# Performance work log

Hardware: AMD Instinct MI355X
Metric: run time of the kernel (lower is better)

The kernel has to match this reference:

```python
import jax, jax.numpy as jnp
import numpy as np

N, A, AD, D, H, KTOP = 5, 900, 8, 256, 8, 300


def _bbox_min_max(anchor):
    # anchor: [N,A,8] = x,y,z,logw,logl,logh,sin_yaw,cos_yaw
    xyz = anchor[..., :3]
    w, l, h = [jnp.exp(anchor[..., i]) for i in (3, 4, 5)]
    sy, cy = anchor[..., 6], anchor[..., 7]
    yaw = jnp.arctan2(sy, cy)
    ca, sa = jnp.abs(jnp.cos(yaw)), jnp.abs(jnp.sin(yaw))
    ex = 0.5 * (l * ca + w * sa)
    ey = 0.5 * (l * sa + w * ca)
    half = jnp.stack([ex, ey, 0.5 * h], axis=-1)
    return xyz - half, xyz + half


def _forward(i2j_anchor, b_anchor, b_feature, transform_matrix, anchor_embed,
             w_roi, b_roi, bn_g, bn_b, fc1_w, fc1_b, fc2_w, fc2_b,
             anc_w, anc_b, lam_w, lam_b, wq, bq, wk, bk, wv, bv, wo, bo,
             ln_g, ln_b, K):
    n, a, ad = b_anchor.shape
    d = b_feature.shape[-1]
    heads = lam_w.shape[-1]
    dh = d // heads
    # ROI scoring + topk selection of anchors to broadcast to neighbors
    roi = jax.nn.sigmoid(b_feature @ w_roi + b_roi)[..., 0]              # [N,A]
    top_scores, top_idx = jax.lax.top_k(roi, K)                          # [N,K]
    conf = top_scores > 0.5                                              # [N,K]
    nbr = jnp.take_along_axis(b_feature, top_idx[..., None], axis=1)     # [N,K,D]
    idx4 = jnp.broadcast_to(top_idx[None, :, :, None], (n, n, K, ad))
    i2j_sel = jnp.take_along_axis(i2j_anchor, idx4, axis=2)              # [N,N,K,AD]
    # remove self (eye-mask): off-diagonal j per row i, row-major order
    offdiag = np.array([[j for j in range(n) if j != i] for i in range(n)])
    rows = np.arange(n)[:, None]
    m = K * (n - 1)
    i2j_rm = i2j_sel[rows, offdiag].reshape(n, m, ad)                    # [N,M,AD]
    tm_rm = transform_matrix[rows, offdiag]                              # [N,N-1,4,4]
    key_feat = nbr[offdiag].reshape(n, m, d)                             # [N,M,D]
    conf_rm = conf[offdiag].reshape(n, m, 1)
    nf_masked = key_feat * conf_rm
    # bbox-range masked aggregation of neighbor features into ego anchors
    mn, mx = _bbox_min_max(b_anchor)                                     # [N,A,3]
    centers = i2j_rm[..., :3]                                            # [N,M,3]
    inside = jnp.all((centers[:, None, :, :] >= mn[:, :, None, :]) &
                     (centers[:, None, :, :] <= mx[:, :, None, :]), axis=-1)  # [N,A,M]
    agg = jnp.einsum('nam,nmd->nad', inside.astype(b_feature.dtype), nf_masked)
    is_greater_than_range = ~jnp.any(inside, axis=1)                     # [N,M]
    b_feature = b_feature + agg
    # transform-matrix encoding: first 3 rows of 4x4 -> BN -> MLP
    mlp_in = tm_rm[:, :, :3, :].reshape(-1, 12)
    mu = mlp_in.mean(0)
    var = mlp_in.var(0)
    xbn = (mlp_in - mu) / jnp.sqrt(var + 1e-5) * bn_g + bn_b
    t = jax.nn.relu(xbn @ fc1_w + fc1_b) @ fc2_w + fc2_b                 # [N*(N-1),D]
    trans_enc = jnp.repeat(t.reshape(n, n - 1, 1, d), K, axis=2).reshape(n, m, d)
    key_pos = i2j_rm @ anc_w + anc_b + trans_enc                         # anchorencoder + trans
    # distance-biased attention mask
    diff = b_anchor[:, :, None, :2] - i2j_rm[:, None, :, :2]
    dist = jnp.sqrt(jnp.sum(diff * diff, axis=-1) + 1e-12)               # cdist [N,A,M]
    lm = (b_feature @ lam_w + lam_b).transpose(0, 2, 1)                  # [N,H,A]
    bias = -jnp.log1p(dist)[:, None, :, :] * lm[..., None]               # [N,H,A,M]
    # multi-head attention (query=b_feature(+anchor_embed pos), key/value=neighbors)
    q = b_feature + anchor_embed
    k = key_feat + key_pos
    v = key_feat
    qh = (q @ wq + bq).reshape(n, a, heads, dh)
    kh = (k @ wk + bk).reshape(n, m, heads, dh)
    vh = (v @ wv + bv).reshape(n, m, heads, dh)
    logits = jnp.einsum('nahd,nmhd->nham', qh, kh) / np.sqrt(dh).astype(np.float32) + bias
    attn = jax.nn.softmax(logits, axis=-1)
    out = jnp.einsum('nham,nmhd->nahd', attn, vh).reshape(n, a, d) @ wo + bo
    res = b_feature + out                                                # residual (identity=query)
    mu2 = res.mean(-1, keepdims=True)
    var2 = res.var(-1, keepdims=True)
    return (res - mu2) / jnp.sqrt(var2 + 1e-5) * ln_g + ln_b


def setup_inputs() -> dict:
    key = jax.random.key(0)
    ks = jax.random.split(key, 24)
    s = 0.05
    inp = {
        'i2j_anchor': jax.random.normal(ks[0], (N, N, A, AD), jnp.float32),
        'b_anchor': jax.random.normal(ks[1], (N, A, AD), jnp.float32),
        'b_feature': jax.random.normal(ks[2], (N, A, D), jnp.float32),
        'transform_matrix': jax.random.normal(ks[3], (N, N, 4, 4), jnp.float32),
        'anchor_embed': jax.random.normal(ks[4], (N, A, D), jnp.float32),
        'w_roi': jax.random.normal(ks[5], (D, 1), jnp.float32) * s,
        'b_roi': jnp.zeros((1,), jnp.float32),
        'bn_g': jnp.ones((12,), jnp.float32),
        'bn_b': jnp.zeros((12,), jnp.float32),
        'fc1_w': jax.random.normal(ks[6], (12, D), jnp.float32) * s,
        'fc1_b': jnp.zeros((D,), jnp.float32),
        'fc2_w': jax.random.normal(ks[7], (D, D), jnp.float32) * s,
        'fc2_b': jnp.zeros((D,), jnp.float32),
        'anc_w': jax.random.normal(ks[8], (AD, D), jnp.float32) * s,
        'anc_b': jnp.zeros((D,), jnp.float32),
        'lam_w': jax.random.normal(ks[9], (D, H), jnp.float32) * s,
        'lam_b': jnp.zeros((H,), jnp.float32),
        'wq': jax.random.normal(ks[10], (D, D), jnp.float32) * s,
        'bq': jnp.zeros((D,), jnp.float32),
        'wk': jax.random.normal(ks[11], (D, D), jnp.float32) * s,
        'bk': jnp.zeros((D,), jnp.float32),
        'wv': jax.random.normal(ks[12], (D, D), jnp.float32) * s,
        'bv': jnp.zeros((D,), jnp.float32),
        'wo': jax.random.normal(ks[13], (D, D), jnp.float32) * s,
        'bo': jnp.zeros((D,), jnp.float32),
        'ln_g': jnp.ones((D,), jnp.float32),
        'ln_b': jnp.zeros((D,), jnp.float32),
        'K': KTOP,
    }
    return inp


def reference(i2j_anchor, b_anchor, b_feature, transform_matrix, anchor_embed,
              w_roi, b_roi, bn_g, bn_b, fc1_w, fc1_b, fc2_w, fc2_b,
              anc_w, anc_b, lam_w, lam_b, wq, bq, wk, bk, wv, bv, wo, bo,
              ln_g, ln_b, K):
    return _forward(i2j_anchor, b_anchor, b_feature, transform_matrix, anchor_embed,
                    w_roi, b_roi, bn_g, bn_b, fc1_w, fc1_b, fc2_w, fc2_b,
                    anc_w, anc_b, lam_w, lam_b, wq, bq, wk, bk, wv, bv, wo, bo,
                    ln_g, ln_b, K)
```

## Files before the change

kernel.cpp:

```cpp
#include <hip/hip_runtime.h>
#include <math.h>

#define N_ 5
#define A_ 900
#define AD_ 8
#define D_ 256
#define H_ 8
#define DH_ 32
#define K_ 300
#define NM1_ 4
#define M_ 1200
#define MP_ 1216
#define KC_ 64
#define HALF_ 600
#define NCHUNK2_ 10

typedef _Float16 f16x8 __attribute__((ext_vector_type(8)));
typedef _Float16 f16x4 __attribute__((ext_vector_type(4)));
typedef float f32x4 __attribute__((ext_vector_type(4)));

__global__ __launch_bounds__(256) void score_kernel(const float* __restrict__ bf,
                                                    const float* __restrict__ w,
                                                    const float* __restrict__ b,
                                                    float* __restrict__ scores) {
  int wid = threadIdx.x >> 6, lane = threadIdx.x & 63;
  int row = blockIdx.x * 4 + wid;
  if (row >= N_ * A_) return;
  const float* x = bf + (long)row * D_;
  float dot = 0.f;
#pragma unroll
  for (int t = 0; t < 4; t++) dot += x[lane + 64 * t] * w[lane + 64 * t];
#pragma unroll
  for (int o = 32; o; o >>= 1) dot += __shfl_xor(dot, o, 64);
  if (lane == 0) scores[row] = 1.0f / (1.0f + expf(-(dot + b[0])));
}

__global__ __launch_bounds__(1024) void topk_kernel(const float* __restrict__ scores,
                                                    int* __restrict__ top_idx,
                                                    float* __restrict__ conf) {
  __shared__ float sc[1024];
  __shared__ int si[1024];
  int i = blockIdx.x, t = threadIdx.x;
  sc[t] = (t < A_) ? scores[i * A_ + t] : -INFINITY;
  si[t] = t;
  __syncthreads();
  for (int k = 2; k <= 1024; k <<= 1) {
    for (int j = k >> 1; j > 0; j >>= 1) {
      int ixj = t ^ j;
      if (ixj > t) {
        bool dir = ((t & k) == 0);
        float a = sc[t], b = sc[ixj];
        bool sw = dir ? (a < b) : (a > b);
        if (sw) {
          sc[t] = b; sc[ixj] = a;
          int tmp = si[t]; si[t] = si[ixj]; si[ixj] = tmp;
        }
      }
      __syncthreads();
    }
  }
  if (t < K_) {
    top_idx[i * K_ + t] = si[t];
    conf[i * K_ + t] = sc[t] > 0.5f ? 1.0f : 0.0f;
  }
}

__global__ __launch_bounds__(256) void mlp_kernel(const float* __restrict__ tm,
                                                  const float* __restrict__ bn_g, const float* __restrict__ bn_b,
                                                  const float* __restrict__ fc1_w, const float* __restrict__ fc1_b,
                                                  const float* __restrict__ fc2_w, const float* __restrict__ fc2_b,
                                                  float* __restrict__ t_out) {
  int r = blockIdx.x;
  int t = threadIdx.x;
  __shared__ float x[20][12];
  __shared__ float y[12];
  __shared__ float hbuf[D_];
  if (t < 240) {
    int rr = t / 12, f = t % 12;
    int i = rr / NM1_, jj = rr % NM1_;
    int j = jj < i ? jj : jj + 1;
    int r4 = f / 4, c4 = f % 4;
    x[rr][f] = tm[((long)(i * N_ + j) * 4 + r4) * 4 + c4];
  }
  __syncthreads();
  if (t < 12) {
    float s = 0.f;
    for (int rr = 0; rr < 20; rr++) s += x[rr][t];
    float m = s / 20.0f;
    float v = 0.f;
    for (int rr = 0; rr < 20; rr++) { float d = x[rr][t] - m; v += d * d; }
    v /= 20.0f;
    y[t] = (x[r][t] - m) * rsqrtf(v + 1e-5f) * bn_g[t] + bn_b[t];
  }
  __syncthreads();
  float acc = fc1_b[t];
#pragma unroll
  for (int f = 0; f < 12; f++) acc += y[f] * fc1_w[f * D_ + t];
  hbuf[t] = fmaxf(acc, 0.0f);
  __syncthreads();
  float acc2 = fc2_b[t];
  for (int k = 0; k < D_; k++) acc2 += hbuf[k] * fc2_w[k * D_ + t];
  t_out[r * D_ + t] = acc2;
}

#define GKT_ 10
__global__ __launch_bounds__(256) void gather_kernel(const float* __restrict__ b_feature,
                                                     const float* __restrict__ i2j_anchor,
                                                     const int* __restrict__ top_idx,
                                                     const float* __restrict__ conf,
                                                     const float* __restrict__ anc_w,
                                                     const float* __restrict__ anc_b,
                                                     const float* __restrict__ t_mlp,
                                                     _Float16* __restrict__ key_feat16,
                                                     float* __restrict__ conf_rm,
                                                     float* __restrict__ i2j_rm,
                                                     _Float16* __restrict__ key_in16) {
  int blk = blockIdx.x;
  int i = blk / NM1_, jj = blk % NM1_;
  int j = jj < i ? jj : jj + 1;
  int k0 = blockIdx.y * GKT_;
  int c = threadIdx.x;
  __shared__ float aw[AD_][D_];
#pragma unroll
  for (int r = 0; r < AD_; r++) aw[r][c] = anc_w[r * D_ + c];
  float ab = anc_b[c];
  float tv = t_mlp[(i * NM1_ + jj) * D_ + c];
  __syncthreads();
  for (int k = k0; k < k0 + GKT_; k++) {
    int idx = top_idx[j * K_ + k];
    float cf = conf[j * K_ + k];
    const float* src = b_feature + ((long)(j * A_ + idx)) * D_;
    float val = src[c];
    long mrow = (long)i * M_ + jj * K_ + k;
    key_feat16[mrow * D_ + c] = (_Float16)val;
    const float* ap = i2j_anchor + ((long)((i * N_ + j) * A_ + idx)) * AD_;
    if (c < AD_) i2j_rm[mrow * AD_ + c] = ap[c];
    if (c == 0) conf_rm[mrow] = cf;
    float pos = ab + tv;
#pragma unroll
    for (int r = 0; r < AD_; r++) pos += ap[r] * aw[r][c];
    key_in16[mrow * D_ + c] = (_Float16)(val + pos);
  }
}

__global__ __launch_bounds__(256) void trans_kernel(const float* __restrict__ w0, const float* __restrict__ w1,
                                                    const float* __restrict__ w2, const float* __restrict__ w3,
                                                    const _Float16* __restrict__ kf,
                                                    _Float16* __restrict__ wT, _Float16* __restrict__ kT) {
  int bid = blockIdx.x;
  int t = threadIdx.x;
  if (bid < 64) {
    int y = bid >> 4, tile = bid & 15;
    const float* src = (y == 0) ? w0 : (y == 1) ? w1 : (y == 2) ? w2 : w3;
    _Float16* dst = wT + (size_t)y * D_ * D_;
    int kr = (tile >> 2) * 64, nc = (tile & 3) * 64;
    __shared__ float lds[64][65];
#pragma unroll
    for (int r = 0; r < 16; r++) {
      int row = r * 4 + (t >> 6), col = t & 63;
      lds[row][col] = src[(size_t)(kr + row) * D_ + nc + col];
    }
    __syncthreads();
#pragma unroll
    for (int r = 0; r < 16; r++) {
      int orow = r * 4 + (t >> 6), ocol = t & 63;
      dst[(size_t)(nc + orow) * D_ + kr + ocol] = (_Float16)lds[ocol][orow];
    }
  } else {
    int b = bid - 64;
    int i = b / 76, rem = b % 76;
    int m0 = (rem % 19) * 64, d0 = (rem / 19) * 64;
    __shared__ _Float16 lds2[64][66];
    const _Float16* src = kf + (size_t)i * M_ * D_;
    _Float16* dst = kT + (size_t)i * D_ * M_;
#pragma unroll
    for (int r = 0; r < 16; r++) {
      int row = r * 4 + (t >> 6), col = t & 63;
      int m = m0 + row;
      lds2[row][col] = (m < M_) ? src[(size_t)m * D_ + d0 + col] : (_Float16)0.0f;
    }
    __syncthreads();
#pragma unroll
    for (int r = 0; r < 16; r++) {
      int orow = r * 4 + (t >> 6), ocol = t & 63;
      int m = m0 + ocol;
      if (m < M_) dst[(size_t)(d0 + orow) * M_ + m] = lds2[ocol][orow];
    }
  }
}

__global__ __launch_bounds__(256) void insbias_kernel(const float* __restrict__ i2j_rm,
                                                      const float* __restrict__ conf_rm,
                                                      const float* __restrict__ ban,
                                                      _Float16* __restrict__ inside,
                                                      _Float16* __restrict__ Lbuf) {
  int i = blockIdx.x;
  int g = blockIdx.y;
  __shared__ float cx[M_], cy[M_], cz[M_], cf[M_];
  for (int m = threadIdx.x; m < M_; m += 256) {
    const float* cp = i2j_rm + ((long)i * M_ + m) * AD_;
    cx[m] = cp[0]; cy[m] = cp[1]; cz[m] = cp[2];
    cf[m] = conf_rm[(long)i * M_ + m];
  }
  __syncthreads();
#pragma unroll
  for (int r = 0; r < 4; r++) {
    int a = g * 4 + r;
    int row = i * A_ + a;
    const float* ap = ban + (long)row * AD_;
    float ax = ap[0], ay = ap[1], az = ap[2];
    float w = expf(ap[3]), l = expf(ap[4]), hh = expf(ap[5]);
    float yaw = atan2f(ap[6], ap[7]);
    float ca = fabsf(cosf(yaw)), sa = fabsf(sinf(yaw));
    float ex = 0.5f * (l * ca + w * sa);
    float ey = 0.5f * (l * sa + w * ca);
    float ez = 0.5f * hh;
    float mn0 = ax - ex, mn1 = ay - ey, mn2 = az - ez;
    float mx0 = ax + ex, mx1 = ay + ey, mx2 = az + ez;
    _Float16* ldst = Lbuf + (size_t)row * MP_;
    _Float16* idst = inside + (size_t)row * M_;
    for (int m = threadIdx.x; m < M_; m += 256) {
      float c0 = cx[m], c1 = cy[m], c2 = cz[m];
      bool ins = (c0 >= mn0) && (c0 <= mx0) && (c1 >= mn1) && (c1 <= mx1) && (c2 >= mn2) && (c2 <= mx2);
      idst[m] = ins ? (_Float16)cf[m] : (_Float16)0.0f;
      float dx = ax - c0, dy = ay - c1;
      ldst[m] = (_Float16)log1pf(sqrtf(dx * dx + dy * dy + 1e-12f));
    }
  }
}

#define GLD_ 74
template <typename TO, bool HAS_BIAS, bool HAS_RES>
__device__ __forceinline__ void gemm_tile_body(
    const _Float16* __restrict__ A, int lda, int Mr,
    const _Float16* __restrict__ B, int ldb,
    const float* __restrict__ bias, const float* __restrict__ res,
    TO* __restrict__ C, int ldc,
    int m0, int n0, int k_begin, int k_end) {
  __shared__ _Float16 As[64 * GLD_];
  __shared__ _Float16 Bs[64 * GLD_];
  int tid = threadIdx.x;
  int lane = tid & 63;
  int wid = tid >> 6;
  int wr = (wid >> 1) * 32, wc = (wid & 1) * 32;
  int lr = lane & 15, lk = (lane >> 4) * 8;
  int srow = tid >> 3;
  int scol = (tid & 7) * 8;
  f16x8 aR[2], bR[2];
  f16x8 zero8 = {};
  auto loadg = [&](int kb) {
#pragma unroll
    for (int r = 0; r < 2; r++) {
      int gm = m0 + srow + r * 32;
      int gk = kb + scol;
      aR[r] = (gm < Mr && gk < k_end) ? *(const f16x8*)&A[(size_t)gm * lda + gk] : zero8;
      int gn = n0 + srow + r * 32;
      bR[r] = (gk < k_end) ? *(const f16x8*)&B[(size_t)gn * ldb + gk] : zero8;
    }
  };
  auto store_lds = [&]() {
#pragma unroll
    for (int r = 0; r < 2; r++) {
      *(f16x8*)&As[(srow + r * 32) * GLD_ + scol] = aR[r];
      *(f16x8*)&Bs[(srow + r * 32) * GLD_ + scol] = bR[r];
    }
  };
  f32x4 acc[2][2] = {};
  int niter = (k_end - k_begin + 63) >> 6;
  loadg(k_begin);
  store_lds();
  __syncthreads();
  for (int it = 0; it < niter; ++it) {
    bool more = (it + 1 < niter);
    if (more) loadg(k_begin + (it + 1) * 64);
#pragma unroll
    for (int ks = 0; ks < 2; ks++) {
      f16x8 af[2], bf[2];
#pragma unroll
      for (int mi = 0; mi < 2; mi++) af[mi] = *(const f16x8*)&As[(wr + mi * 16 + lr) * GLD_ + ks * 32 + lk];
#pragma unroll
      for (int ni = 0; ni < 2; ni++) bf[ni] = *(const f16x8*)&Bs[(wc + ni * 16 + lr) * GLD_ + ks * 32 + lk];
#pragma unroll
      for (int mi = 0; mi < 2; mi++)
#pragma unroll
        for (int ni = 0; ni < 2; ni++)
          acc[mi][ni] = __builtin_amdgcn_mfma_f32_16x16x32_f16(af[mi], bf[ni], acc[mi][ni], 0, 0, 0);
    }
    __syncthreads();
    if (more) { store_lds(); __syncthreads(); }
  }
#pragma unroll
  for (int mi = 0; mi < 2; mi++)
#pragma unroll
    for (int ni = 0; ni < 2; ni++)
#pragma unroll
      for (int rr = 0; rr < 4; rr++) {
        int row = m0 + wr + mi * 16 + (lane >> 4) * 4 + rr;
        int col = n0 + wc + ni * 16 + lr;
        if (row < Mr) {
          float v = acc[mi][ni][rr];
          if (HAS_BIAS) v += bias[col];
          if (HAS_RES) v += res[(size_t)row * ldc + col];
          C[(size_t)row * ldc + col] = (TO)v;
        }
      }
}

__global__ __launch_bounds__(256) void agg_kernel(const _Float16* __restrict__ inside16,
                                                  const _Float16* __restrict__ kT16,
                                                  float* __restrict__ partial) {
  int i = blockIdx.z >> 2, sk = blockIdx.z & 3;
  int kb = sk * 320;
  int ke = kb + 320 < M_ ? kb + 320 : M_;
  gemm_tile_body<float, false, false>(
      inside16 + (size_t)i * A_ * M_, M_, A_,
      kT16 + (size_t)i * D_ * M_, M_,
      nullptr, nullptr,
      partial + (size_t)(sk * N_ + i) * A_ * D_, D_,
      blockIdx.x * 64, blockIdx.y * 64, kb, ke);
}

__global__ __launch_bounds__(256) void agg_reduce(const float* __restrict__ partial,
                                                  const float* __restrict__ b_feature,
                                                  const float* __restrict__ anchor_embed,
                                                  const float* __restrict__ lam_w,
                                                  const float* __restrict__ lam_b,
                                                  float* __restrict__ bf_upd,
                                                  _Float16* __restrict__ qin16,
                                                  float* __restrict__ lm_rm) {
  int wid = threadIdx.x >> 6, lane = threadIdx.x & 63;
  int rg = blockIdx.x * 4 + wid;
  int d0 = lane * 4;
  float lw[4][8];
#pragma unroll
  for (int e = 0; e < 4; e++) {
#pragma unroll
    for (int h = 0; h < 8; h++) lw[e][h] = lam_w[(d0 + e) * 8 + h];
  }
  float4 s = *(const float4*)&partial[(size_t)rg * D_ + d0];
#pragma unroll
  for (int sk = 1; sk < 4; sk++) {
    float4 p = *(const float4*)&partial[((size_t)sk * N_ * A_ + rg) * D_ + d0];
    s.x += p.x; s.y += p.y; s.z += p.z; s.w += p.w;
  }
  float4 bf = *(const float4*)&b_feature[(size_t)rg * D_ + d0];
  s.x += bf.x; s.y += bf.y; s.z += bf.z; s.w += bf.w;
  *(float4*)&bf_upd[(size_t)rg * D_ + d0] = s;
  float4 ae = *(const float4*)&anchor_embed[(size_t)rg * D_ + d0];
  f16x4 q4;
  q4[0] = (_Float16)(s.x + ae.x); q4[1] = (_Float16)(s.y + ae.y);
  q4[2] = (_Float16)(s.z + ae.z); q4[3] = (_Float16)(s.w + ae.w);
  *(f16x4*)&qin16[(size_t)rg * D_ + d0] = q4;
  float sv[4] = {s.x, s.y, s.z, s.w};
  float acc[8] = {};
#pragma unroll
  for (int e = 0; e < 4; e++)
#pragma unroll
    for (int h = 0; h < 8; h++) acc[h] += sv[e] * lw[e][h];
#pragma unroll
  for (int h = 0; h < 8; h++) {
#pragma unroll
    for (int o = 32; o; o >>= 1) acc[h] += __shfl_xor(acc[h], o, 64);
  }
  if (lane == 0) {
#pragma unroll
    for (int h = 0; h < 8; h++) lm_rm[(size_t)rg * H_ + h] = acc[h] + lam_b[h];
  }
}

__global__ __launch_bounds__(256) void qkv_kernel(const _Float16* __restrict__ qA,
                                                  const _Float16* __restrict__ kA,
                                                  const _Float16* __restrict__ vA,
                                                  const _Float16* __restrict__ wT,
                                                  const float* __restrict__ bq,
                                                  const float* __restrict__ bk,
                                                  const float* __restrict__ bv,
                                                  _Float16* __restrict__ qC,
                                                  _Float16* __restrict__ kC,
                                                  _Float16* __restrict__ vC) {
  int bid = blockIdx.x;
  const _Float16 *Ap, *Bp;
  const float* bias;
  _Float16* Cp;
  int Mr, t, mt, nt;
  if (bid < 284)      { Ap = qA; Bp = wT;               bias = bq; Cp = qC; Mr = 4500; t = bid;       mt = t % 71; nt = t / 71; }
  else if (bid < 660) { Ap = kA; Bp = wT + D_ * D_;     bias = bk; Cp = kC; Mr = 6000; t = bid - 284; mt = t % 94; nt = t / 94; }
  else                { Ap = vA; Bp = wT + 2 * D_ * D_; bias = bv; Cp = vC; Mr = 6000; t = bid - 660; mt = t % 94; nt = t / 94; }
  gemm_tile_body<_Float16, true, false>(Ap, D_, Mr, Bp, D_, bias, nullptr, Cp, D_, mt * 64, nt * 64, 0, D_);
}

__global__ __launch_bounds__(256) void outp_kernel(const _Float16* __restrict__ att16,
                                                   const _Float16* __restrict__ woT,
                                                   float* __restrict__ partial2) {
  int bid = blockIdx.x;
  int sk = bid >= 284 ? 1 : 0;
  int t = bid - sk * 284;
  int mt = t % 71, nt = t / 71;
  gemm_tile_body<float, false, false>(att16, D_, 4500, woT, D_, nullptr, nullptr,
                                      partial2 + (size_t)sk * 4500 * D_, D_,
                                      mt * 64, nt * 64, sk * 128, sk * 128 + 128);
}

#define LQP_ 72
#define LKS_ 40
__global__ __launch_bounds__(256) void attn_mfma(const _Float16* __restrict__ qh16,
                                                 const _Float16* __restrict__ kh16,
                                                 const _Float16* __restrict__ vh16,
                                                 const float* __restrict__ lm_rm,
                                                 const _Float16* __restrict__ Lbuf,
                                                 float* __restrict__ part_ms,
                                                 float* __restrict__ part_o) {
  int bid = blockIdx.x;
  int wgid = (bid & 7) * 150 + (bid >> 3);
  int ih = wgid / 30;
  int rest = wgid % 30;
  int half = rest / 15, qt = rest % 15;
  int i = ih >> 3, h = ih & 7;
  int a0 = qt * 64;
  int mbase = half * HALF_;
  int mlimit = mbase + HALF_;

  __shared__ _Float16 QP[64 * LQP_];
  __shared__ _Float16 Ks[64 * LKS_];
  __shared__ _Float16 Vt[32][74];
  __shared__ _Float16 Ls[64 * LQP_];
  __shared__ float lmvs[64];

  int tid = threadIdx.x;
  int lane = tid & 63;
  int w16 = (tid >> 6) * 16;
  int lr = lane & 15;
  int lk = (lane >> 4) * 8;
  int mq = (lane >> 4) * 4;
  int srow = tid >> 2, spiece = tid & 3;
  int lrow = tid >> 3, lpc = (tid & 7) * 8;

  {
    int aq = a0 + srow;
    int a_ld = aq < A_ ? aq : A_ - 1;
    const uint4* src = (const uint4*)(qh16 + ((long)(i * A_ + a_ld) * D_ + h * DH_));
    *(uint4*)&QP[srow * LQP_ + spiece * 8] = src[spiece];
  }
  if (tid < 64) {
    int aq = a0 + tid;
    int a_ld = aq < A_ ? aq : A_ - 1;
    lmvs[tid] = lm_rm[(long)(i * A_ + a_ld) * H_ + h];
  }

  const _Float16* kb = kh16 + (long)i * M_ * D_ + h * DH_;
  const _Float16* vb = vh16 + (long)i * M_ * D_ + h * DH_;
  const _Float16* lptr[2];
#pragma unroll
  for (int rr = 0; rr < 2; rr++) {
    int aq = a0 + lrow + rr * 32;
    int a_ld = aq < A_ ? aq : A_ - 1;
    lptr[rr] = Lbuf + (size_t)(i * A_ + a_ld) * MP_ + lpc;
  }

  uint4 kvR, vvR;
  f16x8 lR[2];
  auto loadr = [&](int c) {
    int m0 = mbase + c * KC_;
    int mrow = m0 + srow;
    if (mrow < M_) {
      kvR = ((const uint4*)(kb + (long)mrow * D_))[spiece];
      vvR = ((const uint4*)(vb + (long)mrow * D_))[spiece];
    } else {
      kvR = make_uint4(0, 0, 0, 0);
      vvR = make_uint4(0, 0, 0, 0);
    }
#pragma unroll
    for (int rr = 0; rr < 2; rr++) lR[rr] = *(const f16x8*)&lptr[rr][m0];
  };

  __syncthreads();

  int qrow = w16 + lr;
  float lmv = lmvs[qrow];
  f16x8 qa = *(const f16x8*)&QP[qrow * LQP_ + lk];

  float m_run = -INFINITY, s_part = 0.0f;
  f32x4 oacc[2] = {};

  loadr(0);

  for (int c = 0; c < NCHUNK2_; c++) {
    int m0 = mbase + c * KC_;
    __syncthreads();
    *(uint4*)&Ks[srow * LKS_ + spiece * 8] = kvR;
    {
      const _Float16* hp = (const _Float16*)&vvR;
#pragma unroll
      for (int e = 0; e < 8; e++) Vt[spiece * 8 + e][srow] = hp[e];
    }
#pragma unroll
    for (int rr = 0; rr < 2; rr++) *(f16x8*)&Ls[(lrow + rr * 32) * LQP_ + lpc] = lR[rr];
    if (c + 1 < NCHUNK2_) loadr(c + 1);
    __syncthreads();

    f32x4 sacc[4];
#pragma unroll
    for (int mb = 0; mb < 4; mb++) {
      f16x8 kf = *(const f16x8*)&Ks[(mb * 16 + lr) * LKS_ + lk];
      sacc[mb] = __builtin_amdgcn_mfma_f32_16x16x32_f16(kf, qa, (f32x4){0.f, 0.f, 0.f, 0.f}, 0, 0, 0);
    }

    float lg[4][4];
#pragma unroll
    for (int mb = 0; mb < 4; mb++) {
      f16x4 l4 = *(const f16x4*)&Ls[qrow * LQP_ + mb * 16 + mq];
#pragma unroll
      for (int rr = 0; rr < 4; rr++) {
        int mcol = m0 + mb * 16 + mq + rr;
        float v = sacc[mb][rr] * 0.17677669529663687f - (float)l4[rr] * lmv;
        lg[mb][rr] = (mcol < mlimit) ? v : -INFINITY;
      }
    }
    float cm = -INFINITY;
#pragma unroll
    for (int mb = 0; mb < 4; mb++)
#pragma unroll
      for (int rr = 0; rr < 4; rr++) cm = fmaxf(cm, lg[mb][rr]);
    cm = fmaxf(cm, __shfl_xor(cm, 16, 64));
    cm = fmaxf(cm, __shfl_xor(cm, 32, 64));
    float nm = fmaxf(m_run, cm);
    float corr = __expf(m_run - nm);
    m_run = nm;
    float ps = 0.0f;
#pragma unroll
    for (int mb = 0; mb < 4; mb++) {
      f16x4 p4;
#pragma unroll
      for (int rr = 0; rr < 4; rr++) {
        float p = __expf(lg[mb][rr] - nm);
        ps += p;
        p4[rr] = (_Float16)p;
      }
      *(f16x4*)&QP[qrow * LQP_ + mb * 16 + mq] = p4;
    }
    s_part = s_part * corr + ps;
#pragma unroll
    for (int r = 0; r < 4; r++) {
      float cr = __shfl(corr, (lane & 48) + mq + r, 64);
      oacc[0][r] *= cr;
      oacc[1][r] *= cr;
    }

#pragma unroll
    for (int ks = 0; ks < 2; ks++) {
      f16x8 pa = *(const f16x8*)&QP[(w16 + lr) * LQP_ + ks * 32 + lk];
#pragma unroll
      for (int db = 0; db < 2; db++) {
        f16x8 vf = *(const f16x8*)&Vt[db * 16 + lr][ks * 32 + lk];
        oacc[db] = __builtin_amdgcn_mfma_f32_16x16x32_f16(pa, vf, oacc[db], 0, 0, 0);
      }
    }
  }

  float st = s_part;
  st += __shfl_xor(st, 16, 64);
  st += __shfl_xor(st, 32, 64);

  size_t base = (size_t)(half * 40 + ih) * A_;
  if (lane < 16) {
    int a = a0 + w16 + lane;
    if (a < A_) {
      part_ms[(base + a) * 2 + 0] = m_run;
      part_ms[(base + a) * 2 + 1] = st;
    }
  }
#pragma unroll
  for (int r = 0; r < 4; r++) {
    int a = a0 + w16 + mq + r;
    if (a < A_) {
      size_t rowb = base + a;
      part_o[rowb * 32 + lr] = oacc[0][r];
      part_o[rowb * 32 + 16 + lr] = oacc[1][r];
    }
  }
}

__global__ __launch_bounds__(256) void attn_merge(const float* __restrict__ part_ms,
                                                  const float* __restrict__ part_o,
                                                  _Float16* __restrict__ att16) {
  int t = threadIdx.x;
  int R = blockIdx.x * 8 + (t >> 5);
  int d = t & 31;
  int ih = R / A_, a = R % A_;
  int i = ih >> 3, h = ih & 7;
  size_t r0 = (size_t)ih * A_ + a;
  size_t r1 = (size_t)(40 + ih) * A_ + a;
  float m0 = part_ms[r0 * 2], s0 = part_ms[r0 * 2 + 1];
  float m1 = part_ms[r1 * 2], s1 = part_ms[r1 * 2 + 1];
  float M = fmaxf(m0, m1);
  float e0 = __expf(m0 - M), e1 = __expf(m1 - M);
  float inv = 1.0f / (s0 * e0 + s1 * e1);
  float o = part_o[r0 * 32 + d] * e0 + part_o[r1 * 32 + d] * e1;
  att16[((size_t)(i * A_ + a)) * D_ + h * DH_ + d] = (_Float16)(o * inv);
}

__global__ __launch_bounds__(256) void ln_kernel(const float* __restrict__ partial2,
                                                 const float* __restrict__ bo,
                                                 const float* __restrict__ resid,
                                                 const float* __restrict__ g,
                                                 const float* __restrict__ b,
                                                 float* __restrict__ out) {
  int row = blockIdx.x;
  int t = threadIdx.x;
  size_t idx = (size_t)row * D_ + t;
  float v = partial2[idx] + partial2[(size_t)4500 * D_ + idx] + bo[t] + resid[idx];
  float s = v, sq = v * v;
#pragma unroll
  for (int o = 32; o; o >>= 1) {
    s += __shfl_xor(s, o, 64);
    sq += __shfl_xor(sq, o, 64);
  }
  __shared__ float ss[4], ssq[4];
  int wid = t >> 6, lane = t & 63;
  if (lane == 0) { ss[wid] = s; ssq[wid] = sq; }
  __syncthreads();
  float ts = ss[0] + ss[1] + ss[2] + ss[3];
  float tq = ssq[0] + ssq[1] + ssq[2] + ssq[3];
  float mean = ts / (float)D_;
  float var = tq / (float)D_ - mean * mean;
  out[idx] = (v - mean) * rsqrtf(var + 1e-5f) * g[t] + b[t];
}

extern "C" void kernel_launch(void* const* d_in, const int* in_sizes, int n_in,
                              void* d_out, int out_size, void* d_ws, size_t ws_size,
                              hipStream_t stream) {
  const float* i2j_anchor   = (const float*)d_in[0];
  const float* b_anchor     = (const float*)d_in[1];
  const float* b_feature    = (const float*)d_in[2];
  const float* tm           = (const float*)d_in[3];
  const float* anchor_embed = (const float*)d_in[4];
  const float* w_roi  = (const float*)d_in[5];
  const float* b_roi  = (const float*)d_in[6];
  const float* bn_g   = (const float*)d_in[7];
  const float* bn_b   = (const float*)d_in[8];
  const float* fc1_w  = (const float*)d_in[9];
  const float* fc1_b  = (const float*)d_in[10];
  const float* fc2_w  = (const float*)d_in[11];
  const float* fc2_b  = (const float*)d_in[12];
  const float* anc_w  = (const float*)d_in[13];
  const float* anc_b  = (const float*)d_in[14];
  const float* lam_w  = (const float*)d_in[15];
  const float* lam_b  = (const float*)d_in[16];
  const float* wq = (const float*)d_in[17];
  const float* bq = (const float*)d_in[18];
  const float* wk = (const float*)d_in[19];
  const float* bk = (const float*)d_in[20];
  const float* wv = (const float*)d_in[21];
  const float* bv = (const float*)d_in[22];
  const float* wo = (const float*)d_in[23];
  const float* bo = (const float*)d_in[24];
  const float* ln_g = (const float*)d_in[25];
  const float* ln_b = (const float*)d_in[26];

  float* ws = (float*)d_ws;
  size_t off = 0;
  auto alloc = [&](size_t n) { float* p = ws + off; off += (n + 3) & ~(size_t)3; return p; };

  float* scores     = alloc(N_ * A_);
  int*   top_idx    = (int*)alloc(N_ * K_);
  float* conf       = alloc(N_ * K_);
  float* t_mlp      = alloc(20 * D_);
  float* conf_rm    = alloc((size_t)N_ * M_);
  float* i2j_rm     = alloc((size_t)N_ * M_ * AD_);
  _Float16* key_feat16 = (_Float16*)alloc((size_t)N_ * M_ * D_ / 2);
  _Float16* key_in16   = (_Float16*)alloc((size_t)N_ * M_ * D_ / 2);
  _Float16* kT16       = (_Float16*)alloc((size_t)N_ * D_ * M_ / 2);
  _Float16* inside16   = (_Float16*)alloc((size_t)N_ * A_ * M_ / 2);
  _Float16* wT16       = (_Float16*)alloc((size_t)4 * D_ * D_ / 2);
  _Float16* Lbuf16     = (_Float16*)alloc((size_t)N_ * A_ * MP_ / 2 + 16);
  float* partial    = alloc((size_t)4 * N_ * A_ * D_);
  float* bf_upd     = alloc((size_t)N_ * A_ * D_);
  _Float16* qin16   = (_Float16*)alloc((size_t)N_ * A_ * D_ / 2);
  _Float16* qh16    = (_Float16*)alloc((size_t)N_ * A_ * D_ / 2);
  _Float16* kh16    = (_Float16*)alloc((size_t)N_ * M_ * D_ / 2);
  _Float16* vh16    = (_Float16*)alloc((size_t)N_ * M_ * D_ / 2);
  float* lm_rm      = alloc((size_t)N_ * A_ * H_);
  _Float16* att16   = (_Float16*)alloc((size_t)N_ * A_ * D_ / 2);
  float* partial2   = alloc((size_t)2 * N_ * A_ * D_);
  float* part_ms    = alloc((size_t)2 * 40 * A_ * 2);
  float* part_o     = alloc((size_t)2 * 40 * A_ * 32);

  score_kernel<<<(N_ * A_ + 3) / 4, 256, 0, stream>>>(b_feature, w_roi, b_roi, scores);
  topk_kernel<<<N_, 1024, 0, stream>>>(scores, top_idx, conf);
  mlp_kernel<<<20, 256, 0, stream>>>(tm, bn_g, bn_b, fc1_w, fc1_b, fc2_w, fc2_b, t_mlp);
  gather_kernel<<<dim3(N_ * NM1_, K_ / GKT_), 256, 0, stream>>>(b_feature, i2j_anchor, top_idx, conf,
                                                                anc_w, anc_b, t_mlp,
                                                                key_feat16, conf_rm, i2j_rm, key_in16);
  trans_kernel<<<64 + 380, 256, 0, stream>>>(wq, wk, wv, wo, key_feat16, wT16, kT16);
  insbias_kernel<<<dim3(N_, A_ / 4), 256, 0, stream>>>(i2j_rm, conf_rm, b_anchor, inside16, Lbuf16);
  agg_kernel<<<dim3(15, 4, N_ * 4), 256, 0, stream>>>(inside16, kT16, partial);
  agg_reduce<<<(N_ * A_) / 4, 256, 0, stream>>>(partial, b_feature, anchor_embed, lam_w, lam_b,
                                                bf_upd, qin16, lm_rm);
  qkv_kernel<<<284 + 376 + 376, 256, 0, stream>>>(qin16, key_in16, key_feat16, wT16,
                                                  bq, bk, bv, qh16, kh16, vh16);
  attn_mfma<<<1200, 256, 0, stream>>>(qh16, kh16, vh16, lm_rm, Lbuf16, part_ms, part_o);
  attn_merge<<<(40 * A_) / 8, 256, 0, stream>>>(part_ms, part_o, att16);
  outp_kernel<<<568, 256, 0, stream>>>(att16, wT16 + 3 * D_ * D_, partial2);
  ln_kernel<<<N_ * A_, 256, 0, stream>>>(partial2, bo, bf_upd, ln_g, ln_b, (float*)d_out);
}
```

Baseline: 179.3 us.

## Write V projection pre-transposed and use exp2 in attention softmax

```diff
diff --git a/kernel.cpp b/kernel.cpp
--- a/kernel.cpp
+++ b/kernel.cpp
@@ -18,6 +18,8 @@
 typedef _Float16 f16x8 __attribute__((ext_vector_type(8)));
 typedef _Float16 f16x4 __attribute__((ext_vector_type(4)));
 typedef float f32x4 __attribute__((ext_vector_type(4)));
+
+#define LOG2E_ 1.4426950408889634f
 
 __global__ __launch_bounds__(256) void score_kernel(const float* __restrict__ bf,
                                                     const float* __restrict__ w,
@@ -230,7 +232,7 @@
 }
 
 #define GLD_ 74
-template <typename TO, bool HAS_BIAS, bool HAS_RES>
+template <typename TO, bool HAS_BIAS, bool HAS_RES, bool VTRANS = false>
 __device__ __forceinline__ void gemm_tile_body(
     const _Float16* __restrict__ A, int lda, int Mr,
     const _Float16* __restrict__ B, int ldb,
@@ -289,6 +291,33 @@
     __syncthreads();
     if (more) { store_lds(); __syncthreads(); }
   }
+  if (VTRANS) {
+#pragma unroll
+    for (int mi = 0; mi < 2; mi++)
+#pragma unroll
+      for (int ni = 0; ni < 2; ni++)
+#pragma unroll
+        for (int rr = 0; rr < 4; rr++) {
+          int ml = wr + mi * 16 + (lane >> 4) * 4 + rr;
+          int dl = wc + ni * 16 + lr;
+          float v = acc[mi][ni][rr];
+          if (HAS_BIAS) v += bias[n0 + dl];
+          As[dl * 72 + ml] = (_Float16)v;
+        }
+    __syncthreads();
+    int dl = tid >> 2, mp = (tid & 3) * 16;
+    int gd = n0 + dl;
+#pragma unroll
+    for (int e8 = 0; e8 < 2; e8++) {
+      int gm = m0 + mp + e8 * 8;
+      if (gm < Mr) {
+        int ii = gm / M_, mm = gm - ii * M_;
+        *(f16x8*)&((_Float16*)C)[(size_t)(ii * D_ + gd) * ldc + mm] =
+            *(const f16x8*)&As[dl * 72 + mp + e8 * 8];
+      }
+    }
+    return;
+  }
 #pragma unroll
   for (int mi = 0; mi < 2; mi++)
 #pragma unroll
@@ -377,16 +406,23 @@
                                                   const float* __restrict__ bv,
                                                   _Float16* __restrict__ qC,
                                                   _Float16* __restrict__ kC,
-                                                  _Float16* __restrict__ vC) {
+                                                  _Float16* __restrict__ vT) {
   int bid = blockIdx.x;
-  const _Float16 *Ap, *Bp;
-  const float* bias;
-  _Float16* Cp;
-  int Mr, t, mt, nt;
-  if (bid < 284)      { Ap = qA; Bp = wT;               bias = bq; Cp = qC; Mr = 4500; t = bid;       mt = t % 71; nt = t / 71; }
-  else if (bid < 660) { Ap = kA; Bp = wT + D_ * D_;     bias = bk; Cp = kC; Mr = 6000; t = bid - 284; mt = t % 94; nt = t / 94; }
-  else                { Ap = vA; Bp = wT + 2 * D_ * D_; bias = bv; Cp = vC; Mr = 6000; t = bid - 660; mt = t % 94; nt = t / 94; }
-  gemm_tile_body<_Float16, true, false>(Ap, D_, Mr, Bp, D_, bias, nullptr, Cp, D_, mt * 64, nt * 64, 0, D_);
+  if (bid < 284) {
+    int mt = bid % 71, nt = bid / 71;
+    gemm_tile_body<_Float16, true, false>(qA, D_, 4500, wT, D_, bq, nullptr, qC, D_,
+                                          mt * 64, nt * 64, 0, D_);
+  } else if (bid < 660) {
+    int t = bid - 284;
+    int mt = t % 94, nt = t / 94;
+    gemm_tile_body<_Float16, true, false>(kA, D_, 6000, wT + D_ * D_, D_, bk, nullptr, kC, D_,
+                                          mt * 64, nt * 64, 0, D_);
+  } else {
+    int t = bid - 660;
+    int mt = t % 94, nt = t / 94;
+    gemm_tile_body<_Float16, true, false, true>(vA, D_, 6000, wT + 2 * D_ * D_, D_, bv, nullptr, vT, MP_,
+                                                mt * 64, nt * 64, 0, D_);
+  }
 }
 
 __global__ __launch_bounds__(256) void outp_kernel(const _Float16* __restrict__ att16,
@@ -405,7 +441,7 @@
 #define LKS_ 40
 __global__ __launch_bounds__(256) void attn_mfma(const _Float16* __restrict__ qh16,
                                                  const _Float16* __restrict__ kh16,
-                                                 const _Float16* __restrict__ vh16,
+                                                 const _Float16* __restrict__ vhT,
                                                  const float* __restrict__ lm_rm,
                                                  const _Float16* __restrict__ Lbuf,
                                                  float* __restrict__ part_ms,
@@ -422,7 +458,7 @@
 
   __shared__ _Float16 QP[64 * LQP_];
   __shared__ _Float16 Ks[64 * LKS_];
-  __shared__ _Float16 Vt[32][74];
+  __shared__ _Float16 Vs[32 * LQP_];
   __shared__ _Float16 Ls[64 * LQP_];
   __shared__ float lmvs[64];
 
@@ -433,7 +469,7 @@
   int lk = (lane >> 4) * 8;
   int mq = (lane >> 4) * 4;
   int srow = tid >> 2, spiece = tid & 3;
-  int lrow = tid >> 3, lpc = (tid & 7) * 8;
+  int vrow = tid >> 3, vpc = (tid & 7) * 8;
 
   {
     int aq = a0 + srow;
@@ -448,27 +484,22 @@
   }
 
   const _Float16* kb = kh16 + (long)i * M_ * D_ + h * DH_;
-  const _Float16* vb = vh16 + (long)i * M_ * D_ + h * DH_;
+  const _Float16* vb = vhT + (size_t)(i * D_ + h * DH_) * MP_;
   const _Float16* lptr[2];
 #pragma unroll
   for (int rr = 0; rr < 2; rr++) {
-    int aq = a0 + lrow + rr * 32;
+    int aq = a0 + vrow + rr * 32;
     int a_ld = aq < A_ ? aq : A_ - 1;
-    lptr[rr] = Lbuf + (size_t)(i * A_ + a_ld) * MP_ + lpc;
-  }
-
-  uint4 kvR, vvR;
-  f16x8 lR[2];
+    lptr[rr] = Lbuf + (size_t)(i * A_ + a_ld) * MP_ + vpc;
+  }
+
+  uint4 kvR;
+  f16x8 vvR, lR[2];
   auto loadr = [&](int c) {
     int m0 = mbase + c * KC_;
     int mrow = m0 + srow;
-    if (mrow < M_) {
-      kvR = ((const uint4*)(kb + (long)mrow * D_))[spiece];
-      vvR = ((const uint4*)(vb + (long)mrow * D_))[spiece];
-    } else {
-      kvR = make_uint4(0, 0, 0, 0);
-      vvR = make_uint4(0, 0, 0, 0);
-    }
+    kvR = (mrow < M_) ? ((const uint4*)(kb + (long)mrow * D_))[spiece] : make_uint4(0, 0, 0, 0);
+    vvR = *(const f16x8*)&vb[(size_t)vrow * MP_ + m0 + vpc];
 #pragma unroll
     for (int rr = 0; rr < 2; rr++) lR[rr] = *(const f16x8*)&lptr[rr][m0];
   };
@@ -476,25 +507,23 @@
   __syncthreads();
 
   int qrow = w16 + lr;
-  float lmv = lmvs[qrow];
+  float lmv2 = lmvs[qrow] * LOG2E_;
   f16x8 qa = *(const f16x8*)&QP[qrow * LQP_ + lk];
 
   float m_run = -INFINITY, s_part = 0.0f;
   f32x4 oacc[2] = {};
 
   loadr(0);
+
+  const float SC2 = 0.17677669529663687f * LOG2E_;
 
   for (int c = 0; c < NCHUNK2_; c++) {
     int m0 = mbase + c * KC_;
     __syncthreads();
     *(uint4*)&Ks[srow * LKS_ + spiece * 8] = kvR;
-    {
-      const _Float16* hp = (const _Float16*)&vvR;
-#pragma unroll
-      for (int e = 0; e < 8; e++) Vt[spiece * 8 + e][srow] = hp[e];
-    }
-#pragma unroll
-    for (int rr = 0; rr < 2; rr++) *(f16x8*)&Ls[(lrow + rr * 32) * LQP_ + lpc] = lR[rr];
+    *(f16x8*)&Vs[vrow * LQP_ + vpc] = vvR;
+#pragma unroll
+    for (int rr = 0; rr < 2; rr++) *(f16x8*)&Ls[(vrow + rr * 32) * LQP_ + vpc] = lR[rr];
     if (c + 1 < NCHUNK2_) loadr(c + 1);
     __syncthreads();
 
@@ -512,7 +541,7 @@
 #pragma unroll
       for (int rr = 0; rr < 4; rr++) {
         int mcol = m0 + mb * 16 + mq + rr;
-        float v = sacc[mb][rr] * 0.17677669529663687f - (float)l4[rr] * lmv;
+        float v = sacc[mb][rr] * SC2 - (float)l4[rr] * lmv2;
         lg[mb][rr] = (mcol < mlimit) ? v : -INFINITY;
       }
     }
@@ -524,7 +553,7 @@
     cm = fmaxf(cm, __shfl_xor(cm, 16, 64));
     cm = fmaxf(cm, __shfl_xor(cm, 32, 64));
     float nm = fmaxf(m_run, cm);
-    float corr = __expf(m_run - nm);
+    float corr = exp2f(m_run - nm);
     m_run = nm;
     float ps = 0.0f;
 #pragma unroll
@@ -532,7 +561,7 @@
       f16x4 p4;
 #pragma unroll
       for (int rr = 0; rr < 4; rr++) {
-        float p = __expf(lg[mb][rr] - nm);
+        float p = exp2f(lg[mb][rr] - nm);
         ps += p;
         p4[rr] = (_Float16)p;
       }
@@ -551,7 +580,7 @@
       f16x8 pa = *(const f16x8*)&QP[(w16 + lr) * LQP_ + ks * 32 + lk];
 #pragma unroll
       for (int db = 0; db < 2; db++) {
-        f16x8 vf = *(const f16x8*)&Vt[db * 16 + lr][ks * 32 + lk];
+        f16x8 vf = *(const f16x8*)&Vs[(db * 16 + lr) * LQP_ + ks * 32 + lk];
         oacc[db] = __builtin_amdgcn_mfma_f32_16x16x32_f16(pa, vf, oacc[db], 0, 0, 0);
       }
     }
@@ -593,7 +622,7 @@
   float m0 = part_ms[r0 * 2], s0 = part_ms[r0 * 2 + 1];
   float m1 = part_ms[r1 * 2], s1 = part_ms[r1 * 2 + 1];
   float M = fmaxf(m0, m1);
-  float e0 = __expf(m0 - M), e1 = __expf(m1 - M);
+  float e0 = exp2f(m0 - M), e1 = exp2f(m1 - M);
   float inv = 1.0f / (s0 * e0 + s1 * e1);
   float o = part_o[r0 * 32 + d] * e0 + part_o[r1 * 32 + d] * e1;
   att16[((size_t)(i * A_ + a)) * D_ + h * DH_ + d] = (_Float16)(o * inv);
@@ -678,7 +707,7 @@
   _Float16* qin16   = (_Float16*)alloc((size_t)N_ * A_ * D_ / 2);
   _Float16* qh16    = (_Float16*)alloc((size_t)N_ * A_ * D_ / 2);
   _Float16* kh16    = (_Float16*)alloc((size_t)N_ * M_ * D_ / 2);
-  _Float16* vh16    = (_Float16*)alloc((size_t)N_ * M_ * D_ / 2);
+  _Float16* vhT16   = (_Float16*)alloc((size_t)N_ * D_ * MP_ / 2 + 16);
   float* lm_rm      = alloc((size_t)N_ * A_ * H_);
   _Float16* att16   = (_Float16*)alloc((size_t)N_ * A_ * D_ / 2);
   float* partial2   = alloc((size_t)2 * N_ * A_ * D_);
@@ -697,8 +726,8 @@
   agg_reduce<<<(N_ * A_) / 4, 256, 0, stream>>>(partial, b_feature, anchor_embed, lam_w, lam_b,
                                                 bf_upd, qin16, lm_rm);
   qkv_kernel<<<284 + 376 + 376, 256, 0, stream>>>(qin16, key_in16, key_feat16, wT16,
-                                                  bq, bk, bv, qh16, kh16, vh16);
-  attn_mfma<<<1200, 256, 0, stream>>>(qh16, kh16, vh16, lm_rm, Lbuf16, part_ms, part_o);
+                                                  bq, bk, bv, qh16, kh16, vhT16);
+  attn_mfma<<<1200, 256, 0, stream>>>(qh16, kh16, vhT16, lm_rm, Lbuf16, part_ms, part_o);
   attn_merge<<<(40 * A_) / 8, 256, 0, stream>>>(part_ms, part_o, att16);
   outp_kernel<<<568, 256, 0, stream>>>(att16, wT16 + 3 * D_ * D_, partial2);
   ln_kernel<<<N_ * A_, 256, 0, stream>>>(partial2, bo, bf_upd, ln_g, ln_b, (float*)d_out);
```

Result: no change. 176.3 us (-1.7%).
